# Kernel optimization log

Measured on AMD Instinct MI355X. Metric: run time of the kernel, lower is better.

Reference implementation:

```python
import jax, jax.numpy as jnp
import numpy as np
from jax import lax

V, D, H, HD, L, E, HID, TOPK, B, T = 32000, 1024, 16, 64, 2, 4, 2048, 2, 1, 1024
EPS = 1e-8


def setup_inputs() -> dict:
    key = jax.random.key(0)
    ks = jax.random.split(key, 10)
    s = 0.02
    so = 0.02 / np.sqrt(2 * L)  # o_proj / down_proj init std
    return dict(
        idx=jax.random.randint(ks[0], (B, T), 0, V),
        tok_emb=jax.random.normal(ks[1], (V, D), jnp.float32) * s,
        attn_norm_w=jnp.ones((L, D), jnp.float32),
        q_w=jax.random.normal(ks[2], (L, D, D), jnp.float32) * s,
        q_b=jnp.zeros((L, D), jnp.float32),
        kv_w=jax.random.normal(ks[3], (L, D, 2 * D), jnp.float32) * s,
        kv_b=jnp.zeros((L, 2 * D), jnp.float32),
        o_w=jax.random.normal(ks[4], (L, D, D), jnp.float32) * so,
        o_b=jnp.zeros((L, D), jnp.float32),
        ffn_norm_w=jnp.ones((L, D), jnp.float32),
        router_w=jax.random.normal(ks[5], (L, D, E), jnp.float32) * s,
        gate_w=jax.random.normal(ks[6], (L, E, D, HID), jnp.float32) * s,
        up_w=jax.random.normal(ks[7], (L, E, D, HID), jnp.float32) * s,
        down_w=jax.random.normal(ks[8], (L, E, HID, D), jnp.float32) * so,
        lnf_w=jnp.ones((D,), jnp.float32),
    )


def _rms(x, w):
    return x / jnp.sqrt(jnp.mean(x * x, axis=-1, keepdims=True) + EPS) * w


def reference(idx, tok_emb, attn_norm_w, q_w, q_b, kv_w, kv_b, o_w, o_b,
              ffn_norm_w, router_w, gate_w, up_w, down_w, lnf_w):
    x = tok_emb[idx]  # [B,T,D]

    # ALiBi bias and causal mask (built once; block_size == T here)
    slopes = jnp.arange(1, H + 1, dtype=jnp.float32) / H          # [H]
    pos = jnp.arange(T, dtype=jnp.float32)
    alibi = slopes[:, None, None] * (pos[None, None, :] - pos[None, :, None])  # [H,T,T]
    causal = jnp.arange(T)[None, :] > jnp.arange(T)[:, None]      # True above diagonal

    for l in range(L):
        # --- causal self-attention with ALiBi ---
        h = _rms(x, attn_norm_w[l])
        q = (h @ q_w[l] + q_b[l]).reshape(B, T, H, HD)
        kv = (h @ kv_w[l] + kv_b[l]).reshape(B, T, 2, H, HD)
        k, v = kv[:, :, 0], kv[:, :, 1]
        att = jnp.einsum('bqhd,bkhd->bhqk', q, k) * (1.0 / np.sqrt(HD))
        att = att + alibi[None]
        att = jnp.where(causal, -jnp.inf, att)
        a = jax.nn.softmax(att, axis=-1)
        y = jnp.einsum('bhqk,bkhd->bqhd', a, v).reshape(B, T, D)
        x = x + y @ o_w[l] + o_b[l]

        # --- MoE FFN (top-k routing, SwiGLU experts, depth-scaled down_proj) ---
        hm = _rms(x, ffn_norm_w[l]).reshape(B * T, D)             # [N,D]
        rlog = hm @ router_w[l]                                   # [N,E]
        vals, sel = lax.top_k(rlog, TOPK)                         # [N,K]
        w = jax.nn.softmax(vals.astype(jnp.float32), axis=-1).astype(hm.dtype)
        # dense per-expert compute, combined sparsely via routing weights
        g = jax.nn.silu(jnp.einsum('nd,edh->enh', hm, gate_w[l])) \
            * jnp.einsum('nd,edh->enh', hm, up_w[l])              # [E,N,HID]
        out_e = jnp.einsum('enh,ehd->end', g, down_w[l]) * (1.0 / np.sqrt(l + 1))
        combine = jnp.sum(jax.nn.one_hot(sel, E, dtype=hm.dtype) * w[..., None], axis=1)  # [N,E]
        moe = jnp.einsum('ne,end->nd', combine, out_e).reshape(B, T, D)
        x = x + moe

    logits = _rms(x, lnf_w) @ tok_emb.T  # tied head weight
    return logits
```

## Files before the change

kernel.cpp:

```cpp
#include <hip/hip_runtime.h>
#include <cmath>

typedef __attribute__((ext_vector_type(8))) _Float16 f16x8;
typedef __attribute__((ext_vector_type(8))) unsigned short u16x8;
typedef __attribute__((ext_vector_type(4))) float f32x4;

#define DEV static __device__ __forceinline__

constexpr int Dm   = 1024;
constexpr int HIDm = 2048;
constexpr int NT   = 1024;
constexpr int NV   = 32000;
constexpr float EPSf  = 1e-8f;
constexpr float LOSC  = 4096.0f;
constexpr float ILOSC = 1.0f / 4096.0f;

DEV unsigned short h2u(_Float16 h){ union{_Float16 h; unsigned short u;} v; v.h=h; return v.u; }

DEV f32x4 MF(f16x8 a, f16x8 b, f32x4 c){ return __builtin_amdgcn_mfma_f32_16x16x32_f16(a,b,c,0,0,0); }

typedef __attribute__((address_space(1))) void GV;
typedef __attribute__((address_space(3))) void LV;
DEV void gll16(const void* g, void* l){
  __builtin_amdgcn_global_load_lds((GV*)(__UINTPTR_TYPE__)g, (LV*)l, 16, 0, 0);
}

DEV int swk(int lane){ return (((lane&3) ^ ((lane>>3)&3))*8); }
DEV int rdc(int fr, int fg){ return ((fg ^ ((fr>>1)&3))*8); }

template<int SPLIT>
DEV void st_sp(unsigned short* __restrict__ hi, unsigned short* __restrict__ lo, size_t o, float v){
  _Float16 hh = (_Float16)v;
  hi[o] = h2u(hh);
  if constexpr (SPLIT==3) lo[o] = h2u((_Float16)((v - (float)hh)*LOSC));
}

__global__ __launch_bounds__(256) void k_init(
    const int* __restrict__ idx, const float* __restrict__ emb,
    float* __restrict__ x, unsigned short* __restrict__ emb16, int gbase)
{
  const int b = blockIdx.x;
  if (b < gbase){
    const size_t i = ((size_t)b*256 + threadIdx.x)*8;
    const float4 v0 = *(const float4*)&emb[i];
    const float4 v1 = *(const float4*)&emb[i+4];
    u16x8 h;
    h[0]=h2u((_Float16)v0.x); h[1]=h2u((_Float16)v0.y);
    h[2]=h2u((_Float16)v0.z); h[3]=h2u((_Float16)v0.w);
    h[4]=h2u((_Float16)v1.x); h[5]=h2u((_Float16)v1.y);
    h[6]=h2u((_Float16)v1.z); h[7]=h2u((_Float16)v1.w);
    *(u16x8*)&emb16[i] = h;
  } else {
    const int t = b - gbase;
    const int d = threadIdx.x*4;
    *(float4*)&x[(size_t)t*Dm + d] = *(const float4*)&emb[(size_t)idx[t]*Dm + d];
  }
}

template<int SPLIT>
__global__ __launch_bounds__(256) void k_rms(
    const float* __restrict__ x, const float* __restrict__ w,
    unsigned short* __restrict__ ohi, unsigned short* __restrict__ olo)
{
  const int t = blockIdx.x, tid = threadIdx.x;
  const float* row = x + (size_t)t*Dm;
  float s = 0.f;
  #pragma unroll
  for (int i=0;i<4;++i){ const float v = row[tid + i*256]; s += v*v; }
  #pragma unroll
  for (int d=1; d<64; d<<=1) s += __shfl_xor(s, d);
  __shared__ float red[4];
  if ((tid&63)==0) red[tid>>6] = s;
  __syncthreads();
  const float tot = red[0]+red[1]+red[2]+red[3];
  const float rstd = rsqrtf(tot*(1.0f/Dm) + EPSf);
  #pragma unroll
  for (int i=0;i<4;++i){
    const int c = tid + i*256;
    st_sp<SPLIT>(ohi, olo, (size_t)t*Dm + c, row[c]*rstd*w[c]);
  }
}

template<int SPLIT>
__global__ __launch_bounds__(256) void k_fuse_o(
    const float* __restrict__ part, const float* __restrict__ ob,
    const float* __restrict__ fnw, const float* __restrict__ rw,
    float* __restrict__ x, unsigned short* __restrict__ hhi,
    unsigned short* __restrict__ hlo, float* __restrict__ cmb)
{
  const int t = blockIdx.x, tid = threadIdx.x, wv = tid>>6, lane = tid&63;
  const int c = tid*4;
  float4 s = *(float4*)&x[(size_t)t*Dm + c];
  #pragma unroll
  for (int z=0; z<4; ++z){
    const float4 p = *(const float4*)&part[((size_t)z*NT + t)*Dm + c];
    s.x+=p.x; s.y+=p.y; s.z+=p.z; s.w+=p.w;
  }
  const float4 b4 = *(const float4*)&ob[c];
  s.x+=b4.x; s.y+=b4.y; s.z+=b4.z; s.w+=b4.w;
  *(float4*)&x[(size_t)t*Dm + c] = s;

  float ss = s.x*s.x + s.y*s.y + s.z*s.z + s.w*s.w;
  #pragma unroll
  for (int d=1; d<64; d<<=1) ss += __shfl_xor(ss, d);
  __shared__ float red[4];
  if (lane==0) red[wv] = ss;
  __syncthreads();
  const float rstd = rsqrtf((red[0]+red[1]+red[2]+red[3])*(1.0f/Dm) + EPSf);

  const float4 w4 = *(const float4*)&fnw[c];
  const float sv[4] = {s.x,s.y,s.z,s.w};
  const float wv4[4] = {w4.x,w4.y,w4.z,w4.w};
  float hm[4];
  float lg[4] = {0.f,0.f,0.f,0.f};
  #pragma unroll
  for (int j=0;j<4;++j){
    hm[j] = sv[j]*rstd*wv4[j];
    st_sp<SPLIT>(hhi, hlo, (size_t)t*Dm + c + j, hm[j]);
    const float4 r4 = *(const float4*)&rw[(size_t)(c+j)*4];
    lg[0] += hm[j]*r4.x; lg[1] += hm[j]*r4.y; lg[2] += hm[j]*r4.z; lg[3] += hm[j]*r4.w;
  }
  #pragma unroll
  for (int d=1; d<64; d<<=1){
    lg[0]+=__shfl_xor(lg[0],d); lg[1]+=__shfl_xor(lg[1],d);
    lg[2]+=__shfl_xor(lg[2],d); lg[3]+=__shfl_xor(lg[3],d);
  }
  __shared__ float red2[4][4];
  if (lane==0){ red2[wv][0]=lg[0]; red2[wv][1]=lg[1]; red2[wv][2]=lg[2]; red2[wv][3]=lg[3]; }
  __syncthreads();
  if (tid==0){
    float L[4];
    #pragma unroll
    for (int e=0;e<4;++e) L[e] = red2[0][e]+red2[1][e]+red2[2][e]+red2[3][e];
    int s0 = 0;
    for (int e=1;e<4;++e) if (L[e] > L[s0]) s0 = e;
    int s1 = -1;
    for (int e=0;e<4;++e){ if (e==s0) continue; if (s1<0 || L[e] > L[s1]) s1 = e; }
    const float eb2 = expf(L[s1] - L[s0]);
    const float inv = 1.0f/(1.0f + eb2);
    float o[4] = {0.f,0.f,0.f,0.f};
    o[s0] = inv; o[s1] = eb2*inv;
    cmb[t*4+0]=o[0]; cmb[t*4+1]=o[1]; cmb[t*4+2]=o[2]; cmb[t*4+3]=o[3];
  }
}

__global__ __launch_bounds__(256) void k_fuse_moe(
    const float* __restrict__ part, const float* __restrict__ cmb,
    const float* __restrict__ w, float* __restrict__ x,
    unsigned short* __restrict__ dst, int writex)
{
  const int t = blockIdx.x, tid = threadIdx.x, wv = tid>>6, lane = tid&63;
  const int c = tid*4;
  float4 s = *(float4*)&x[(size_t)t*Dm + c];
  #pragma unroll
  for (int e=0; e<4; ++e){
    if (cmb[(size_t)t*4 + e] > 0.f){
      const float4 p0 = *(const float4*)&part[((size_t)(e*2+0)*NT + t)*Dm + c];
      const float4 p1 = *(const float4*)&part[((size_t)(e*2+1)*NT + t)*Dm + c];
      s.x+=p0.x+p1.x; s.y+=p0.y+p1.y; s.z+=p0.z+p1.z; s.w+=p0.w+p1.w;
    }
  }
  if (writex) *(float4*)&x[(size_t)t*Dm + c] = s;
  float ss = s.x*s.x + s.y*s.y + s.z*s.z + s.w*s.w;
  #pragma unroll
  for (int d=1; d<64; d<<=1) ss += __shfl_xor(ss, d);
  __shared__ float red[4];
  if (lane==0) red[wv] = ss;
  __syncthreads();
  const float rstd = rsqrtf((red[0]+red[1]+red[2]+red[3])*(1.0f/Dm) + EPSf);
  const float4 w4 = *(const float4*)&w[c];
  const float sv[4] = {s.x,s.y,s.z,s.w};
  const float wv4[4] = {w4.x,w4.y,w4.z,w4.w};
  #pragma unroll
  for (int j=0;j<4;++j)
    dst[(size_t)t*Dm + c + j] = h2u((_Float16)(sv[j]*rstd*wv4[j]));
}

__global__ __launch_bounds__(256) void k_scan(
    const float* __restrict__ cmb, int* __restrict__ tl,
    float* __restrict__ cwl, int* __restrict__ cnt)
{
  const int e = threadIdx.x>>6, lane = threadIdx.x&63;
  int base = 0;
  for (int t0=0; t0<NT; t0+=64){
    const float w = cmb[(size_t)(t0+lane)*4 + e];
    const unsigned long long m = __ballot(w > 0.f);
    const int pre = __popcll(m & ((1ull<<lane)-1ull));
    if (w > 0.f){ tl[e*NT + base + pre] = t0+lane; cwl[e*NT + base + pre] = w; }
    base += __popcll(m);
  }
  if (lane==0) cnt[e] = base;
}

template<int SPLIT>
DEV void wconv_tile(const float* __restrict__ W, unsigned short* __restrict__ Whi,
                    unsigned short* __restrict__ Wlo, int K, int N, int n0, int k0,
                    float (*tile)[65], int t)
{
  const int r = t>>2;
  #pragma unroll
  for (int i=0;i<4;++i){
    const int c = (t&3)*16 + i*4;
    *(float4*)&tile[r][c] = *(const float4*)&W[(size_t)(k0+r)*N + n0 + c];
  }
  __syncthreads();
  const int n = t>>2;
  #pragma unroll
  for (int i=0;i<2;++i){
    const int kc = (t&3)*8 + i*32;
    u16x8 hi, lo;
    #pragma unroll
    for (int j=0;j<8;++j){
      const float v = tile[kc+j][n];
      const _Float16 hh = (_Float16)v;
      hi[j] = h2u(hh);
      if constexpr (SPLIT==3) lo[j] = h2u((_Float16)((v-(float)hh)*LOSC));
      else lo[j] = 0;
    }
    *(u16x8*)&Whi[(size_t)(n0+n)*K + k0 + kc] = hi;
    if constexpr (SPLIT==3) *(u16x8*)&Wlo[(size_t)(n0+n)*K + k0 + kc] = lo;
  }
}

template<int SPLIT>
__global__ __launch_bounds__(256) void k_wconv(
    const float* __restrict__ W, unsigned short* __restrict__ Whi,
    unsigned short* __restrict__ Wlo, int K, int N)
{
  __shared__ float tile[64][65];
  const size_t eb = (size_t)blockIdx.z * (size_t)K * N;
  wconv_tile<SPLIT>(W + eb, Whi + eb, Wlo + eb, K, N, blockIdx.x*64, blockIdx.y*64,
                    tile, threadIdx.x);
}

template<int SPLIT>
__global__ __launch_bounds__(256) void k_wconv_qkvo(
    const float* __restrict__ qw, const float* __restrict__ kvw, const float* __restrict__ ow,
    unsigned short* __restrict__ Wh, unsigned short* __restrict__ Wl,
    unsigned short* __restrict__ WOh, unsigned short* __restrict__ WOl)
{
  __shared__ float tile[64][65];
  const int b = blockIdx.x, t = threadIdx.x;
  if (b < 256){
    wconv_tile<SPLIT>(qw, Wh, Wl, Dm, Dm, (b&15)*64, (b>>4)*64, tile, t);
  } else if (b < 768){
    const int c = b - 256;
    wconv_tile<SPLIT>(kvw, Wh + (size_t)Dm*Dm, Wl + (size_t)Dm*Dm,
                      Dm, 2*Dm, (c&31)*64, (c>>5)*64, tile, t);
  } else {
    const int c = b - 768;
    wconv_tile<SPLIT>(ow, WOh, WOl, Dm, Dm, (c&15)*64, (c>>4)*64, tile, t);
  }
}

template<int SPLIT>
__global__ __launch_bounds__(256) void k_wconv_gu(
    const float* __restrict__ gw, const float* __restrict__ uw,
    unsigned short* __restrict__ WGh, unsigned short* __restrict__ WGl,
    unsigned short* __restrict__ WUh, unsigned short* __restrict__ WUl)
{
  __shared__ float tile[64][65];
  const int b = blockIdx.x, t = threadIdx.x;
  const int half = b >> 11;
  const int c = b & 2047;
  const int e = c >> 9, cc = c & 511;
  const size_t eb = (size_t)e * (size_t)Dm * HIDm;
  const int n0 = (cc&31)*64, k0 = (cc>>5)*64;
  if (half == 0)
    wconv_tile<SPLIT>(gw + eb, WGh + eb, WGl + eb, Dm, HIDm, n0, k0, tile, t);
  else
    wconv_tile<SPLIT>(uw + eb, WUh + eb, WUl + eb, Dm, HIDm, n0, k0, tile, t);
}

template<int SPLIT, int ZMODE>
__global__ __launch_bounds__(256) void k_mm(
    const unsigned short* __restrict__ Ahi, const unsigned short* __restrict__ Alo,
    const unsigned short* __restrict__ Bhi, const unsigned short* __restrict__ Blo,
    float* __restrict__ part, int lda, int ldb, int K, int ldo)
{
  constexpr int PL = (SPLIT==3)?2:1;
  __shared__ __align__(16) unsigned short As[PL][128][32];
  __shared__ __align__(16) unsigned short Bs[PL][128][32];
  const int tid=threadIdx.x, wv=tid>>6, lane=tid&63, fr=lane&15, fg=lane>>4;
  const int n0=blockIdx.x*128, r0=blockIdx.y*128, zz=blockIdx.z;
  const int wr=(wv>>1)*64, wc=(wv&1)*64;
  const int sr=lane>>2, sk=swk(lane);
  const int rc = rdc(fr, fg);

  const f32x4 z4={0.f,0.f,0.f,0.f};
  f32x4 accM[4][4], accC[4][4];
  #pragma unroll
  for (int i=0;i<4;++i)
    #pragma unroll
    for (int j=0;j<4;++j){ accM[i][j]=z4; accC[i][j]=z4; }

  for (int kt=0; kt<K; kt+=32){
    #pragma unroll
    for (int i=0;i<2;++i){
      const int rr = wv*32 + i*16 + sr;
      size_t ao, bo;
      if constexpr (ZMODE==2){
        ao = (size_t)(r0+rr)*lda + zz*K + kt + sk;
        bo = (size_t)(n0+rr)*ldb + zz*K + kt + sk;
      } else {
        ao = (size_t)(r0+rr)*lda + kt + sk;
        bo = (size_t)(n0+rr)*ldb + kt + sk;
      }
      gll16(&Ahi[ao], &As[0][wv*32+i*16][0]);
      if constexpr (SPLIT==3) gll16(&Alo[ao], &As[1][wv*32+i*16][0]);
      gll16(&Bhi[bo], &Bs[0][wv*32+i*16][0]);
      if constexpr (SPLIT==3) gll16(&Blo[bo], &Bs[1][wv*32+i*16][0]);
    }
    __syncthreads();
    f16x8 a[4][PL], b[4][PL];
    #pragma unroll
    for (int rt=0;rt<4;++rt)
      #pragma unroll
      for (int p=0;p<PL;++p) a[rt][p] = *(const f16x8*)&As[p][wr+rt*16+fr][rc];
    #pragma unroll
    for (int ct=0;ct<4;++ct)
      #pragma unroll
      for (int p=0;p<PL;++p) b[ct][p] = *(const f16x8*)&Bs[p][wc+ct*16+fr][rc];
    #pragma unroll
    for (int rt=0;rt<4;++rt)
      #pragma unroll
      for (int ct=0;ct<4;++ct){
        accM[rt][ct] = MF(a[rt][0], b[ct][0], accM[rt][ct]);
        if constexpr (SPLIT==3){
          accC[rt][ct] = MF(a[rt][0], b[ct][1], accC[rt][ct]);
          accC[rt][ct] = MF(a[rt][1], b[ct][0], accC[rt][ct]);
        }
      }
    __syncthreads();
  }

  #pragma unroll
  for (int rt=0;rt<4;++rt)
    #pragma unroll
    for (int ct=0;ct<4;++ct)
      #pragma unroll
      for (int j=0;j<4;++j){
        const int row = r0 + wr + rt*16 + fg*4 + j;
        const int col = n0 + wc + ct*16 + fr;
        float v = accM[rt][ct][j];
        if constexpr (SPLIT==3) v += accC[rt][ct][j]*ILOSC;
        part[((size_t)zz*NT + row)*ldo + col] = v;
      }
}

template<int SPLIT>
__global__ __launch_bounds__(256) void k_comb_qkvt(
    const float* __restrict__ part, const float* __restrict__ qb, const float* __restrict__ kvb,
    unsigned short* __restrict__ qhi, unsigned short* __restrict__ qlo,
    unsigned short* __restrict__ khi, unsigned short* __restrict__ klo,
    unsigned short* __restrict__ vthi, unsigned short* __restrict__ vtlo)
{
  __shared__ float tile[64][65];
  const int bid = blockIdx.x, tid = threadIdx.x;
  if (bid < 1024){
    const int t = bid;
    #pragma unroll
    for (int i=0;i<2;++i){
      const int col = tid*4 + i*1024;
      const float4 p0 = *(const float4*)&part[(size_t)t*3072 + col];
      const float4 p1 = *(const float4*)&part[((size_t)NT + t)*3072 + col];
      float v[4] = {p0.x+p1.x, p0.y+p1.y, p0.z+p1.z, p0.w+p1.w};
      #pragma unroll
      for (int j=0;j<4;++j){
        const int c = col + j;
        if (c < Dm) st_sp<SPLIT>(qhi, qlo, (size_t)t*Dm + c, v[j] + qb[c]);
        else        st_sp<SPLIT>(khi, klo, (size_t)t*Dm + (c-Dm), v[j] + kvb[c-Dm]);
      }
    }
  } else {
    const int c = bid - 1024;
    const int d0 = (c&15)*64, t0 = (c>>4)*64;
    {
      const int tl_ = tid>>2, dc = (tid&3)*16;
      #pragma unroll
      for (int i=0;i<4;++i){
        const int d = dc + i*4;
        const float4 p0 = *(const float4*)&part[(size_t)(t0+tl_)*3072 + 2048 + d0 + d];
        const float4 p1 = *(const float4*)&part[((size_t)NT + t0+tl_)*3072 + 2048 + d0 + d];
        tile[tl_][d+0] = p0.x+p1.x + kvb[1024+d0+d+0];
        tile[tl_][d+1] = p0.y+p1.y + kvb[1024+d0+d+1];
        tile[tl_][d+2] = p0.z+p1.z + kvb[1024+d0+d+2];
        tile[tl_][d+3] = p0.w+p1.w + kvb[1024+d0+d+3];
      }
    }
    __syncthreads();
    #pragma unroll
    for (int i=0;i<2;++i){
      const int u = tid + i*256;
      const int dl = u>>3, tch = (u&7)*8;
      u16x8 hi, lo;
      #pragma unroll
      for (int j=0;j<8;++j){
        const float v = tile[tch+j][dl];
        const _Float16 hh = (_Float16)v;
        hi[j] = h2u(hh);
        if constexpr (SPLIT==3) lo[j] = h2u((_Float16)((v-(float)hh)*LOSC));
        else lo[j] = 0;
      }
      *(u16x8*)&vthi[(size_t)(d0+dl)*NT + t0 + tch] = hi;
      if constexpr (SPLIT==3) *(u16x8*)&vtlo[(size_t)(d0+dl)*NT + t0 + tch] = lo;
    }
  }
}

template<int SPLIT>
__global__ __launch_bounds__(256) void k_down(
    const unsigned short* __restrict__ Ahi, const unsigned short* __restrict__ Alo,
    const unsigned short* __restrict__ Bhi, const unsigned short* __restrict__ Blo,
    const int* __restrict__ tl, const int* __restrict__ cnt,
    float* __restrict__ part)
{
  constexpr int PL = (SPLIT==3)?2:1;
  const int zz = blockIdx.z, e = zz>>1, ks = zz&1;
  const int r0 = blockIdx.y*128, n0 = blockIdx.x*128;
  const int cn = cnt[e];
  if (r0 >= cn) return;
  __shared__ __align__(16) unsigned short As[PL][128][32];
  __shared__ __align__(16) unsigned short Bs[PL][128][32];
  __shared__ int tl_s[128];
  const int tid=threadIdx.x, wv=tid>>6, lane=tid&63, fr=lane&15, fg=lane>>4;
  const int wr=(wv>>1)*64, wc=(wv&1)*64;
  const int sr=lane>>2, sk=swk(lane);
  const int rc = rdc(fr, fg);
  if (tid < 128) tl_s[tid] = (r0+tid < cn) ? tl[e*NT + r0 + tid] : -1;

  const f32x4 z4={0.f,0.f,0.f,0.f};
  f32x4 accM[4][4], accC[4][4];
  #pragma unroll
  for (int i=0;i<4;++i)
    #pragma unroll
    for (int j=0;j<4;++j){ accM[i][j]=z4; accC[i][j]=z4; }

  const int kbeg = ks*1024, kend = kbeg + 1024;
  for (int kt=kbeg; kt<kend; kt+=32){
    #pragma unroll
    for (int i=0;i<2;++i){
      const int rr = wv*32 + i*16 + sr;
      const size_t ao = (size_t)((e<<10) + r0 + rr)*HIDm + kt + sk;
      const size_t bo = (size_t)e*((size_t)Dm*HIDm) + (size_t)(n0+rr)*HIDm + kt + sk;
      gll16(&Ahi[ao], &As[0][wv*32+i*16][0]);
      if constexpr (SPLIT==3) gll16(&Alo[ao], &As[1][wv*32+i*16][0]);
      gll16(&Bhi[bo], &Bs[0][wv*32+i*16][0]);
      if constexpr (SPLIT==3) gll16(&Blo[bo], &Bs[1][wv*32+i*16][0]);
    }
    __syncthreads();
    f16x8 a[4][PL], b[4][PL];
    #pragma unroll
    for (int rt=0;rt<4;++rt)
      #pragma unroll
      for (int p=0;p<PL;++p) a[rt][p] = *(const f16x8*)&As[p][wr+rt*16+fr][rc];
    #pragma unroll
    for (int ct=0;ct<4;++ct)
      #pragma unroll
      for (int p=0;p<PL;++p) b[ct][p] = *(const f16x8*)&Bs[p][wc+ct*16+fr][rc];
    #pragma unroll
    for (int rt=0;rt<4;++rt)
      #pragma unroll
      for (int ct=0;ct<4;++ct){
        accM[rt][ct] = MF(a[rt][0], b[ct][0], accM[rt][ct]);
        if constexpr (SPLIT==3){
          accC[rt][ct] = MF(a[rt][0], b[ct][1], accC[rt][ct]);
          accC[rt][ct] = MF(a[rt][1], b[ct][0], accC[rt][ct]);
        }
      }
    __syncthreads();
  }

  #pragma unroll
  for (int rt=0;rt<4;++rt)
    #pragma unroll
    for (int ct=0;ct<4;++ct)
      #pragma unroll
      for (int j=0;j<4;++j){
        const int i = wr + rt*16 + fg*4 + j;
        const int col = n0 + wc + ct*16 + fr;
        float v = accM[rt][ct][j];
        if constexpr (SPLIT==3) v += accC[rt][ct][j]*ILOSC;
        const int tok = tl_s[i];
        if (tok >= 0) part[((size_t)zz*NT + tok)*Dm + col] = v;
      }
}

template<int SPLIT>
__global__ __launch_bounds__(512) void k_guf(
    const unsigned short* __restrict__ Ahi, const unsigned short* __restrict__ Alo,
    const unsigned short* __restrict__ Ghi, const unsigned short* __restrict__ Glo,
    const unsigned short* __restrict__ Uhi, const unsigned short* __restrict__ Ulo,
    const int* __restrict__ tl, const float* __restrict__ cwl, const int* __restrict__ cnt,
    unsigned short* __restrict__ Hhi, unsigned short* __restrict__ Hlo, float scale)
{
  constexpr int PL=(SPLIT==3)?2:1;
  const int e = blockIdx.z, r0 = blockIdx.y*128, n0 = blockIdx.x*64;
  const int cn = cnt[e];
  if (r0 >= cn) return;
  __shared__ __align__(16) unsigned short As[PL][128][32];
  __shared__ __align__(16) unsigned short Gs[PL][64][32];
  __shared__ __align__(16) unsigned short Us[PL][64][32];
  __shared__ float cw_s[128];
  const int tid=threadIdx.x, wv=tid>>6, lane=tid&63, fr=lane&15, fg=lane>>4;
  const int wr=(wv>>1)*32, wc=(wv&1)*32;
  const int sr=lane>>2, sk=swk(lane);
  const int rc = rdc(fr, fg);
  const size_t ebW = (size_t)e * ((size_t)HIDm*Dm);
  if (tid < 128) cw_s[tid] = (r0+tid < cn) ? cwl[e*NT + r0 + tid]*scale : 0.f;

  const int lrA = r0 + wv*16 + sr;
  const int tokA = tl[e*NT + (lrA < cn ? lrA : cn-1)];
  const size_t abase = (size_t)tokA*Dm + sk;
  const int rrB = (wv&3)*16 + sr;
  const size_t bbase = ebW + (size_t)(n0+rrB)*Dm + sk;

  const f32x4 z4={0.f,0.f,0.f,0.f};
  f32x4 aGM[2][2],aGC[2][2],aUM[2][2],aUC[2][2];
  #pragma unroll
  for (int i=0;i<2;++i)
    #pragma unroll
    for (int j=0;j<2;++j){ aGM[i][j]=z4; aGC[i][j]=z4; aUM[i][j]=z4; aUC[i][j]=z4; }

  for (int kt=0; kt<Dm; kt+=32){
    gll16(&Ahi[abase + kt], &As[0][wv*16][0]);
    if constexpr (SPLIT==3) gll16(&Alo[abase + kt], &As[1][wv*16][0]);
    if (wv < 4){
      gll16(&Ghi[bbase + kt], &Gs[0][(wv&3)*16][0]);
      if constexpr (SPLIT==3) gll16(&Glo[bbase + kt], &Gs[1][(wv&3)*16][0]);
    } else {
      gll16(&Uhi[bbase + kt], &Us[0][(wv&3)*16][0]);
      if constexpr (SPLIT==3) gll16(&Ulo[bbase + kt], &Us[1][(wv&3)*16][0]);
    }
    __syncthreads();
    f16x8 a[2][PL], bg[2][PL], bu[2][PL];
    #pragma unroll
    for (int rt=0;rt<2;++rt)
      #pragma unroll
      for (int p=0;p<PL;++p) a[rt][p] = *(const f16x8*)&As[p][wr+rt*16+fr][rc];
    #pragma unroll
    for (int ct=0;ct<2;++ct)
      #pragma unroll
      for (int p=0;p<PL;++p){
        bg[ct][p] = *(const f16x8*)&Gs[p][wc+ct*16+fr][rc];
        bu[ct][p] = *(const f16x8*)&Us[p][wc+ct*16+fr][rc];
      }
    #pragma unroll
    for (int rt=0;rt<2;++rt)
      #pragma unroll
      for (int ct=0;ct<2;++ct){
        aGM[rt][ct] = MF(a[rt][0], bg[ct][0], aGM[rt][ct]);
        aUM[rt][ct] = MF(a[rt][0], bu[ct][0], aUM[rt][ct]);
        if constexpr (SPLIT==3){
          aGC[rt][ct] = MF(a[rt][0], bg[ct][1], aGC[rt][ct]);
          aGC[rt][ct] = MF(a[rt][1], bg[ct][0], aGC[rt][ct]);
          aUC[rt][ct] = MF(a[rt][0], bu[ct][1], aUC[rt][ct]);
          aUC[rt][ct] = MF(a[rt][1], bu[ct][0], aUC[rt][ct]);
        }
      }
    __syncthreads();
  }
  #pragma unroll
  for (int rt=0;rt<2;++rt)
    #pragma unroll
    for (int ct=0;ct<2;++ct)
      #pragma unroll
      for (int j=0;j<4;++j){
        const int i = wr + rt*16 + fg*4 + j;
        const int row = r0 + i;
        const int col = n0 + wc + ct*16 + fr;
        float g2 = aGM[rt][ct][j], u = aUM[rt][ct][j];
        if constexpr (SPLIT==3){ g2 += aGC[rt][ct][j]*ILOSC; u += aUC[rt][ct][j]*ILOSC; }
        const float cw = cw_s[i];
        const float h = (g2/(1.0f + expf(-g2))) * u * cw;
        st_sp<SPLIT>(Hhi, Hlo, (size_t)((e<<10) + row)*HIDm + col, h);
      }
}

__global__ __launch_bounds__(256) void k_lg(
    const unsigned short* __restrict__ Ahi, const float* __restrict__ emb,
    float* __restrict__ out)
{
  __shared__ __align__(16) unsigned short As[128][32];
  __shared__ __align__(16) unsigned short Bs[128][32];
  const int tid=threadIdx.x, wv=tid>>6, lane=tid&63, fr=lane&15, fg=lane>>4;
  const int w = (blockIdx.x & 7)*250 + (blockIdx.x >> 3);
  const int n0 = (w>>3)*128, r0 = (w&7)*128;
  const int wr=(wv>>1)*64, wc=(wv&1)*64;
  const int sr=lane>>2, sk=swk(lane);
  const int rc = rdc(fr, fg);
  const int br = tid>>1;
  const f32x4 z4={0.f,0.f,0.f,0.f};
  f32x4 acc[4][4];
  #pragma unroll
  for (int i=0;i<4;++i)
    #pragma unroll
    for (int j=0;j<4;++j) acc[i][j]=z4;

  for (int kt=0; kt<Dm; kt+=32){
    #pragma unroll
    for (int i=0;i<2;++i){
      const int rr = wv*32 + i*16 + sr;
      gll16(&Ahi[(size_t)(r0+rr)*Dm + kt + sk], &As[wv*32+i*16][0]);
    }
    {
      const int bc = (tid&1)*16;
      const float* s = &emb[(size_t)(n0+br)*Dm + kt + bc];
      const float4 v0 = *(const float4*)s;
      const float4 v1 = *(const float4*)(s+4);
      const float4 v2 = *(const float4*)(s+8);
      const float4 v3 = *(const float4*)(s+12);
      u16x8 h0, h1;
      h0[0]=h2u((_Float16)v0.x); h0[1]=h2u((_Float16)v0.y);
      h0[2]=h2u((_Float16)v0.z); h0[3]=h2u((_Float16)v0.w);
      h0[4]=h2u((_Float16)v1.x); h0[5]=h2u((_Float16)v1.y);
      h0[6]=h2u((_Float16)v1.z); h0[7]=h2u((_Float16)v1.w);
      h1[0]=h2u((_Float16)v2.x); h1[1]=h2u((_Float16)v2.y);
      h1[2]=h2u((_Float16)v2.z); h1[3]=h2u((_Float16)v2.w);
      h1[4]=h2u((_Float16)v3.x); h1[5]=h2u((_Float16)v3.y);
      h1[6]=h2u((_Float16)v3.z); h1[7]=h2u((_Float16)v3.w);
      const int s_ = (br>>1)&3;
      const int u0 = (tid&1)*2;
      *(u16x8*)&Bs[br][(u0^s_)*8]     = h0;
      *(u16x8*)&Bs[br][((u0+1)^s_)*8] = h1;
    }
    __syncthreads();
    f16x8 a[4], b[4];
    #pragma unroll
    for (int rt=0;rt<4;++rt) a[rt] = *(const f16x8*)&As[wr+rt*16+fr][rc];
    #pragma unroll
    for (int ct=0;ct<4;++ct) b[ct] = *(const f16x8*)&Bs[wc+ct*16+fr][rc];
    #pragma unroll
    for (int rt=0;rt<4;++rt)
      #pragma unroll
      for (int ct=0;ct<4;++ct) acc[rt][ct] = MF(a[rt], b[ct], acc[rt][ct]);
    __syncthreads();
  }
  #pragma unroll
  for (int rt=0;rt<4;++rt)
    #pragma unroll
    for (int ct=0;ct<4;++ct)
      #pragma unroll
      for (int j=0;j<4;++j)
        out[(size_t)(r0+wr+rt*16+fg*4+j)*NV + n0+wc+ct*16+fr] = acc[rt][ct][j];
}

__global__ __launch_bounds__(512) void k_lg16(
    const unsigned short* __restrict__ Ahi, const unsigned short* __restrict__ B16,
    float* __restrict__ out)
{
  __shared__ __align__(16) unsigned short As[256][64];
  __shared__ __align__(16) unsigned short Bs[256][64];
  const int tid=threadIdx.x, wv=tid>>6, lane=tid&63, fr=lane&15, fg=lane>>4;
  const int xcd = blockIdx.x & 7, ii = blockIdx.x >> 3;
  const int w = (xcd < 4 ? xcd*63 : 252 + (xcd-4)*62) + ii;
  const int n0 = (w>>2)*256, r0 = (w&3)*256;
  const int wrow=(wv>>2)*128, wcol=(wv&3)*64;
  const int srow = lane>>3;
  const int sk = (((lane&7) ^ srow)*8);
  const f32x4 z4={0.f,0.f,0.f,0.f};
  f32x4 acc[8][4];
  #pragma unroll
  for (int i=0;i<8;++i)
    #pragma unroll
    for (int j=0;j<4;++j) acc[i][j]=z4;

  for (int kt=0; kt<Dm; kt+=64){
    #pragma unroll
    for (int i=0;i<4;++i){
      const int rr = wv*32 + i*8 + srow;
      gll16(&Ahi[(size_t)(r0+rr)*Dm + kt + sk], &As[wv*32+i*8][0]);
      gll16(&B16[(size_t)(n0+rr)*Dm + kt + sk], &Bs[wv*32+i*8][0]);
    }
    __syncthreads();
    #pragma unroll
    for (int kk=0;kk<2;++kk){
      f16x8 a[8], b[4];
      #pragma unroll
      for (int rt=0;rt<8;++rt)
        a[rt] = *(const f16x8*)&As[wrow+rt*16+fr][(((kk*4+fg) ^ (fr&7))*8)];
      #pragma unroll
      for (int ct=0;ct<4;++ct)
        b[ct] = *(const f16x8*)&Bs[wcol+ct*16+fr][(((kk*4+fg) ^ (fr&7))*8)];
      #pragma unroll
      for (int rt=0;rt<8;++rt)
        #pragma unroll
        for (int ct=0;ct<4;++ct) acc[rt][ct] = MF(a[rt], b[ct], acc[rt][ct]);
    }
    __syncthreads();
  }
  #pragma unroll
  for (int rt=0;rt<8;++rt)
    #pragma unroll
    for (int ct=0;ct<4;++ct)
      #pragma unroll
      for (int j=0;j<4;++j)
        out[(size_t)(r0+wrow+rt*16+fg*4+j)*NV + n0+wcol+ct*16+fr] = acc[rt][ct][j];
}

template<int SPLIT>
__global__ __launch_bounds__(64) void k_attn(
    const unsigned short* __restrict__ qhi, const unsigned short* __restrict__ qlo,
    const unsigned short* __restrict__ khi, const unsigned short* __restrict__ klo,
    const unsigned short* __restrict__ vthi, const unsigned short* __restrict__ vtlo,
    unsigned short* __restrict__ yhi, unsigned short* __restrict__ ylo)
{
  constexpr int PL = (SPLIT==3) ? 2 : 1;
  const int qt = blockIdx.x, hd = blockIdx.y;
  const int lane = threadIdx.x;
  const int fr = lane&15, fg = lane>>4;
  const int rbase = qt*16;
  const float slope = (float)(hd+1) * (1.0f/16.0f);

  __shared__ __align__(16) unsigned short Ps[PL][16][32];

  f16x8 aq[2][PL];
  #pragma unroll
  for (int c=0;c<2;++c){
    const size_t off = (size_t)(rbase+fr)*Dm + hd*64 + c*32 + fg*8;
    aq[c][0] = *(const f16x8*)&qhi[off];
    if constexpr (SPLIT==3) aq[c][1] = *(const f16x8*)&qlo[off];
  }

  const f32x4 z4 = {0.f,0.f,0.f,0.f};
  f32x4 yM[4], yC[4];
  #pragma unroll
  for (int ct=0;ct<4;++ct){ yM[ct]=z4; yC[ct]=z4; }
  float m[4], lsum[4];
  #pragma unroll
  for (int j=0;j<4;++j){ m[j] = -INFINITY; lsum[j] = 0.f; }

  const int nkt = qt/2 + 1;
  for (int kt=0; kt<nkt; ++kt){
    f32x4 sM[2], sC[2];
    sM[0]=z4; sM[1]=z4; sC[0]=z4; sC[1]=z4;
    #pragma unroll
    for (int kh=0; kh<2; ++kh){
      #pragma unroll
      for (int c=0;c<2;++c){
        const size_t off = (size_t)(kt*32 + kh*16 + fr)*Dm + hd*64 + c*32 + fg*8;
        const f16x8 b0 = *(const f16x8*)&khi[off];
        sM[kh] = MF(aq[c][0], b0, sM[kh]);
        if constexpr (SPLIT==3){
          const f16x8 b1 = *(const f16x8*)&klo[off];
          sC[kh] = MF(aq[c][0], b1, sC[kh]);
          sC[kh] = MF(aq[c][1], b0, sC[kh]);
        }
      }
    }
    float sv[2][4], mx[4];
    #pragma unroll
    for (int j=0;j<4;++j) mx[j] = -INFINITY;
    #pragma unroll
    for (int kh=0; kh<2; ++kh)
      #pragma unroll
      for (int j=0;j<4;++j){
        const int kcol = kt*32 + kh*16 + fr;
        const int row  = rbase + fg*4 + j;
        float s = sM[kh][j];
        if constexpr (SPLIT==3) s += sC[kh][j]*ILOSC;
        s = s*0.125f + slope*(float)(kcol - row);
        sv[kh][j] = (kcol > row) ? -INFINITY : s;
        mx[j] = fmaxf(mx[j], sv[kh][j]);
      }
    #pragma unroll
    for (int d=1; d<16; d<<=1)
      #pragma unroll
      for (int j=0;j<4;++j) mx[j] = fmaxf(mx[j], __shfl_xor(mx[j], d));
    float resc[4];
    #pragma unroll
    for (int j=0;j<4;++j){
      const float mn = fmaxf(m[j], mx[j]);
      resc[j] = expf(m[j] - mn);
      m[j] = mn;
    }
    float p[2][4], psum[4];
    #pragma unroll
    for (int j=0;j<4;++j) psum[j] = 0.f;
    #pragma unroll
    for (int kh=0;kh<2;++kh)
      #pragma unroll
      for (int j=0;j<4;++j){
        const float pv = (sv[kh][j] == -INFINITY) ? 0.f : expf(sv[kh][j] - m[j]);
        p[kh][j] = pv; psum[j] += pv;
      }
    #pragma unroll
    for (int d=1; d<16; d<<=1)
      #pragma unroll
      for (int j=0;j<4;++j) psum[j] += __shfl_xor(psum[j], d);
    #pragma unroll
    for (int j=0;j<4;++j) lsum[j] = lsum[j]*resc[j] + psum[j];
    #pragma unroll
    for (int ct=0;ct<4;++ct)
      #pragma unroll
      for (int j=0;j<4;++j){ yM[ct][j]*=resc[j]; yC[ct][j]*=resc[j]; }
    #pragma unroll
    for (int kh=0;kh<2;++kh)
      #pragma unroll
      for (int j=0;j<4;++j){
        const float pv = p[kh][j];
        _Float16 ph = (_Float16)pv;
        Ps[0][fg*4+j][kh*16+fr] = h2u(ph);
        if constexpr (SPLIT==3)
          Ps[1][fg*4+j][kh*16+fr] = h2u((_Float16)((pv-(float)ph)*LOSC));
      }
    asm volatile("s_waitcnt lgkmcnt(0)" ::: "memory");
    f16x8 pa[PL];
    pa[0] = *(const f16x8*)&Ps[0][fr][fg*8];
    if constexpr (SPLIT==3) pa[1] = *(const f16x8*)&Ps[1][fr][fg*8];
    #pragma unroll
    for (int ct=0;ct<4;++ct){
      const size_t off = (size_t)(hd*64 + ct*16 + fr)*NT + kt*32 + fg*8;
      const f16x8 v0 = *(const f16x8*)&vthi[off];
      yM[ct] = MF(pa[0], v0, yM[ct]);
      if constexpr (SPLIT==3){
        const f16x8 v1 = *(const f16x8*)&vtlo[off];
        yC[ct] = MF(pa[0], v1, yC[ct]);
        yC[ct] = MF(pa[1], v0, yC[ct]);
      }
    }
    asm volatile("s_waitcnt lgkmcnt(0)" ::: "memory");
  }
  #pragma unroll
  for (int ct=0;ct<4;++ct)
    #pragma unroll
    for (int j=0;j<4;++j){
      float v = yM[ct][j];
      if constexpr (SPLIT==3) v += yC[ct][j]*ILOSC;
      v /= lsum[j];
      const size_t off = (size_t)(rbase + fg*4 + j)*Dm + hd*64 + ct*16 + fr;
      st_sp<SPLIT>(yhi, ylo, off, v);
    }
}

struct Ptrs {
  float* x; float* cmb; float* part; float* cwl; int* tl; int* cnt;
  unsigned short *hhi,*hlo,*qhi,*qlo,*khi,*klo,*vthi,*vtlo,*yhi,*ylo,*Hhi,*Hlo;
  unsigned short *Wqkvh,*Wqkvl,*WOh,*WOl,*WGh,*WGl,*WUh,*WUl,*WDh,*WDl;
};

template<int S>
static void run_layer(const Ptrs& P, int l,
    const float* anw, const float* qw, const float* qb, const float* kvw, const float* kvb,
    const float* ow, const float* ob, const float* fnw, const float* rw,
    const float* gw, const float* uw, const float* dw,
    const float* nextw, unsigned short* nextdst, int writex, float scale, hipStream_t stream)
{
  (void)anw;
  k_wconv_qkvo<S><<<dim3(1024), dim3(256), 0, stream>>>(
      qw + (size_t)l*Dm*Dm, kvw + (size_t)l*Dm*2*Dm, ow + (size_t)l*Dm*Dm,
      P.Wqkvh, P.Wqkvl, P.WOh, P.WOl);
  k_mm<S,2><<<dim3(24,8,2), dim3(256), 0, stream>>>(P.hhi, P.hlo, P.Wqkvh, P.Wqkvl,
      P.part, Dm, Dm, 512, 3072);
  k_comb_qkvt<S><<<dim3(1280), dim3(256), 0, stream>>>(P.part, qb + l*Dm, kvb + l*2*Dm,
      P.qhi, P.qlo, P.khi, P.klo, P.vthi, P.vtlo);
  k_attn<S><<<dim3(64,16), dim3(64), 0, stream>>>(P.qhi,P.qlo,P.khi,P.klo,P.vthi,P.vtlo,P.yhi,P.ylo);
  k_mm<S,2><<<dim3(8,8,4), dim3(256), 0, stream>>>(P.yhi, P.ylo, P.WOh, P.WOl,
      P.part, Dm, Dm, 256, Dm);
  k_fuse_o<S><<<dim3(NT), dim3(256), 0, stream>>>(P.part, ob + l*Dm, fnw + l*Dm,
      rw + (size_t)l*Dm*4, P.x, P.hhi, P.hlo, P.cmb);
  k_scan<<<dim3(1), dim3(256), 0, stream>>>(P.cmb, P.tl, P.cwl, P.cnt);
  k_wconv_gu<S><<<dim3(4096), dim3(256), 0, stream>>>(
      gw + (size_t)l*4*Dm*HIDm, uw + (size_t)l*4*Dm*HIDm, P.WGh, P.WGl, P.WUh, P.WUl);
  k_guf<S><<<dim3(32,8,4), dim3(512), 0, stream>>>(P.hhi, P.hlo, P.WGh, P.WGl, P.WUh, P.WUl,
      P.tl, P.cwl, P.cnt, P.Hhi, P.Hlo, scale);
  k_wconv<S><<<dim3(16,32,4), dim3(256), 0, stream>>>(dw + (size_t)l*4*HIDm*Dm, P.WDh, P.WDl, HIDm, Dm);
  k_down<S><<<dim3(8,8,8), dim3(256), 0, stream>>>(P.Hhi, P.Hlo, P.WDh, P.WDl,
      P.tl, P.cnt, P.part);
  k_fuse_moe<<<dim3(NT), dim3(256), 0, stream>>>(P.part, P.cmb, nextw, P.x, nextdst, writex);
}

extern "C" void kernel_launch(void* const* d_in, const int* in_sizes, int n_in,
                              void* d_out, int out_size, void* d_ws, size_t ws_size,
                              hipStream_t stream)
{
  (void)in_sizes; (void)n_in; (void)out_size;
  const int*   idx = (const int*)d_in[0];
  const float* emb = (const float*)d_in[1];
  const float* anw = (const float*)d_in[2];
  const float* qw  = (const float*)d_in[3];
  const float* qb  = (const float*)d_in[4];
  const float* kvw = (const float*)d_in[5];
  const float* kvb = (const float*)d_in[6];
  const float* ow  = (const float*)d_in[7];
  const float* ob  = (const float*)d_in[8];
  const float* fnw = (const float*)d_in[9];
  const float* rw  = (const float*)d_in[10];
  const float* gw  = (const float*)d_in[11];
  const float* uw  = (const float*)d_in[12];
  const float* dw  = (const float*)d_in[13];
  const float* lnf = (const float*)d_in[14];

  constexpr size_t MB = (size_t)1<<20;
  constexpr size_t KB = (size_t)1<<10;
  char* sc = (char*)d_out;
  Ptrs P;
  P.x     = (float*)sc;
  P.hhi   = (unsigned short*)(sc + 4*MB);
  P.hlo   = (unsigned short*)(sc + 6*MB);
  P.qhi   = (unsigned short*)(sc + 8*MB);
  P.qlo   = (unsigned short*)(sc + 10*MB);
  P.khi   = (unsigned short*)(sc + 12*MB);
  P.klo   = (unsigned short*)(sc + 14*MB);
  P.vthi  = (unsigned short*)(sc + 16*MB);
  P.vtlo  = (unsigned short*)(sc + 18*MB);
  P.yhi   = (unsigned short*)(sc + 20*MB);
  P.ylo   = (unsigned short*)(sc + 22*MB);
  P.cmb   = (float*)(sc + 24*MB);
  P.tl    = (int*)(sc + 24*MB + 64*KB);
  P.cwl   = (float*)(sc + 24*MB + 128*KB);
  P.cnt   = (int*)(sc + 24*MB + 192*KB);
  P.Hhi   = (unsigned short*)(sc + 25*MB);
  P.Hlo   = (unsigned short*)(sc + 41*MB);
  P.Wqkvh = (unsigned short*)(sc + 57*MB);
  P.Wqkvl = (unsigned short*)(sc + 63*MB);
  P.WOh   = (unsigned short*)(sc + 69*MB);
  P.WOl   = (unsigned short*)(sc + 71*MB);
  P.WGh   = (unsigned short*)(sc + 57*MB);
  P.WGl   = (unsigned short*)(sc + 73*MB);
  P.WUh   = (unsigned short*)(sc + 89*MB);
  P.WUl   = (unsigned short*)(sc + 105*MB);
  P.WDh   = (unsigned short*)(sc + 57*MB);
  P.WDl   = (unsigned short*)(sc + 73*MB);
  P.part  = (float*)(sc + 89*MB);
  unsigned short* xhat  = (unsigned short*)d_ws;
  unsigned short* emb16 = (unsigned short*)((char*)d_ws + 2*MB);
  const bool big_ws = ws_size >= 68*MB;
  float* out = (float*)d_out;

  const int gbase = big_ws ? 16000 : 0;
  k_init<<<dim3(gbase + NT), dim3(256), 0, stream>>>(idx, emb, P.x, emb16, gbase);
  k_rms<3><<<dim3(NT), dim3(256), 0, stream>>>(P.x, anw, P.hhi, P.hlo);

  run_layer<3>(P, 0, anw, qw, qb, kvw, kvb, ow, ob, fnw, rw, gw, uw, dw,
               anw + Dm, P.hhi, 1, 1.0f, stream);
  run_layer<1>(P, 1, anw, qw, qb, kvw, kvb, ow, ob, fnw, rw, gw, uw, dw,
               lnf, xhat, 0, 0.70710678f, stream);

  if (big_ws)
    k_lg16<<<dim3(500), dim3(512), 0, stream>>>(xhat, emb16, out);
  else
    k_lg<<<dim3(2000), dim3(256), 0, stream>>>(xhat, emb, out);
}
```

Baseline: 785.7 us.

## Double-buffer LDS tiles in the logits GEMM with K-step of 32

```diff
diff --git a/kernel.cpp b/kernel.cpp
--- a/kernel.cpp
+++ b/kernel.cpp
@@ -649,15 +649,16 @@
     const unsigned short* __restrict__ Ahi, const unsigned short* __restrict__ B16,
     float* __restrict__ out)
 {
-  __shared__ __align__(16) unsigned short As[256][64];
-  __shared__ __align__(16) unsigned short Bs[256][64];
+  __shared__ __align__(16) unsigned short As[2][256][32];
+  __shared__ __align__(16) unsigned short Bs[2][256][32];
   const int tid=threadIdx.x, wv=tid>>6, lane=tid&63, fr=lane&15, fg=lane>>4;
   const int xcd = blockIdx.x & 7, ii = blockIdx.x >> 3;
   const int w = (xcd < 4 ? xcd*63 : 252 + (xcd-4)*62) + ii;
   const int n0 = (w>>2)*256, r0 = (w&3)*256;
   const int wrow=(wv>>2)*128, wcol=(wv&3)*64;
-  const int srow = lane>>3;
-  const int sk = (((lane&7) ^ srow)*8);
+  const int sr = wv*16 + (lane>>2);
+  const int sk = swk(lane);
+  const int rc = rdc(fr, fg);
   const f32x4 z4={0.f,0.f,0.f,0.f};
   f32x4 acc[8][4];
   #pragma unroll
@@ -665,30 +666,36 @@
     #pragma unroll
     for (int j=0;j<4;++j) acc[i][j]=z4;
 
-  for (int kt=0; kt<Dm; kt+=64){
-    #pragma unroll
-    for (int i=0;i<4;++i){
-      const int rr = wv*32 + i*8 + srow;
-      gll16(&Ahi[(size_t)(r0+rr)*Dm + kt + sk], &As[wv*32+i*8][0]);
-      gll16(&B16[(size_t)(n0+rr)*Dm + kt + sk], &Bs[wv*32+i*8][0]);
-    }
+  auto stage = [&](int bb, int kt){
+    #pragma unroll
+    for (int i=0;i<2;++i){
+      gll16(&Ahi[(size_t)(r0 + i*128 + sr)*Dm + kt + sk], &As[bb][i*128 + wv*16][0]);
+      gll16(&B16[(size_t)(n0 + i*128 + sr)*Dm + kt + sk], &Bs[bb][i*128 + wv*16][0]);
+    }
+  };
+  auto compute = [&](int bb){
+    f16x8 a[8], b[4];
+    #pragma unroll
+    for (int rt=0;rt<8;++rt) a[rt] = *(const f16x8*)&As[bb][wrow+rt*16+fr][rc];
+    #pragma unroll
+    for (int ct=0;ct<4;++ct) b[ct] = *(const f16x8*)&Bs[bb][wcol+ct*16+fr][rc];
+    #pragma unroll
+    for (int rt=0;rt<8;++rt)
+      #pragma unroll
+      for (int ct=0;ct<4;++ct) acc[rt][ct] = MF(a[rt], b[ct], acc[rt][ct]);
+  };
+
+  stage(0, 0);
+  __syncthreads();
+  int cur = 0;
+  for (int kt=32; kt<Dm; kt+=32){
+    stage(cur^1, kt);
+    compute(cur);
     __syncthreads();
-    #pragma unroll
-    for (int kk=0;kk<2;++kk){
-      f16x8 a[8], b[4];
-      #pragma unroll
-      for (int rt=0;rt<8;++rt)
-        a[rt] = *(const f16x8*)&As[wrow+rt*16+fr][(((kk*4+fg) ^ (fr&7))*8)];
-      #pragma unroll
-      for (int ct=0;ct<4;++ct)
-        b[ct] = *(const f16x8*)&Bs[wcol+ct*16+fr][(((kk*4+fg) ^ (fr&7))*8)];
-      #pragma unroll
-      for (int rt=0;rt<8;++rt)
-        #pragma unroll
-        for (int ct=0;ct<4;++ct) acc[rt][ct] = MF(a[rt], b[ct], acc[rt][ct]);
-    }
-    __syncthreads();
-  }
+    cur ^= 1;
+  }
+  compute(cur);
+
   #pragma unroll
   for (int rt=0;rt<8;++rt)
     #pragma unroll
```

Result: no change. 799.3 us (+1.7%).
